# Kernel optimization log

Measured on AMD Instinct MI355X. Metric: run time of the kernel, lower is better.

Reference implementation:

```python
import jax, jax.numpy as jnp
import numpy as np

def setup_inputs() -> dict:
    key = jax.random.key(0)
    k1, k2, k3 = jax.random.split(key, 3)
    shape = (2, 2048, 8, 64)  # [n, l, h, d]
    return {
        "q": jax.random.normal(k1, shape, dtype=jnp.float32),
        "k": jax.random.normal(k2, shape, dtype=jnp.float32),
        "v": jax.random.normal(k3, shape, dtype=jnp.float32),
    }

def reference(q, k, v):
    # QK^T: [n, l, s, h]
    qk = jnp.einsum('nlhd,nshd->nlsh', q, k)
    softmax_temp = 1.0 / (q.shape[3] ** 0.5)
    attn = jax.nn.softmax(softmax_temp * qk, axis=2)
    # weighted values: [n, l, h, d]
    return jnp.einsum('nlsh,nshd->nlhd', attn, v)
```

## Files before the change

### kernel.cpp

```cpp
#include <hip/hip_runtime.h>
#include <hip/hip_bf16.h>
#include <math.h>

typedef float floatx16 __attribute__((ext_vector_type(16)));
typedef __bf16 bf16x8 __attribute__((ext_vector_type(8)));

#define SEQ 2048
#define NH 8
#define DH 64
#define NB 2
#define HEADS 16
#define HSTRIDE (SEQ * DH)
#define TILE_E (64 * 64)

__device__ __forceinline__ unsigned short f2bf(float x) {
  union { __bf16 b; unsigned short u; } c; c.b = (__bf16)x; return c.u;
}
__device__ __forceinline__ unsigned int pk2bf(float a, float b) {
  union { __hip_bfloat162 h2; unsigned int u; } c;
  c.h2 = __float22bfloat162_rn(make_float2(a, b));
  return c.u;
}

__device__ __forceinline__ void hswap_fwd(unsigned& a, unsigned& b) {
  asm volatile("v_permlane32_swap_b32 %0, %1" : "+v"(a), "+v"(b));
}
__device__ __forceinline__ void hswap_rev(unsigned& a, unsigned& b) {
  asm volatile("v_permlane32_swap_b32 %0, %1" : "+v"(b), "+v"(a));
}

__global__ __launch_bounds__(256)
void pack_kv(const float* __restrict__ k, const float* __restrict__ v,
             unsigned short* __restrict__ kb, unsigned short* __restrict__ vb) {
  __shared__ unsigned short Ts[64][68];
  const int tid  = threadIdx.x;
  const int bx   = blockIdx.x;
  const int head = bx & 15;
  const int kt   = bx >> 4;
  const int n = head >> 3, h = head & 7;

  #pragma unroll
  for (int j2 = 0; j2 < 2; ++j2) {
    int c = j2 * 256 + tid;
    int lane = c & 63;
    int kk = (c >> 6) & 3, ks2 = c >> 8;
    int row = kt * 64 + ks2 * 32 + (lane & 31);
    int d0  = kk * 16 + (lane >> 5) * 8;
    const float* src = k + ((size_t)(n * SEQ + row) * NH + h) * DH + d0;
    float4 a = *(const float4*)src;
    float4 b = *(const float4*)(src + 4);
    ushort4 lo, hi;
    lo.x = f2bf(a.x); lo.y = f2bf(a.y); lo.z = f2bf(a.z); lo.w = f2bf(a.w);
    hi.x = f2bf(b.x); hi.y = f2bf(b.y); hi.z = f2bf(b.z); hi.w = f2bf(b.w);
    unsigned short* dst = kb + (size_t)head * HSTRIDE + kt * TILE_E + c * 8;
    *(ushort4*)dst = lo;
    *(ushort4*)(dst + 4) = hi;
  }

  #pragma unroll
  for (int i = 0; i < 4; ++i) {
    int id = i * 256 + tid;
    int s  = id >> 4;
    int c4 = (id & 15) * 4;
    size_t g = ((size_t)((n * SEQ + kt * 64 + s) * NH + h)) * DH + c4;
    float4 x = *(const float4*)(v + g);
    ushort4 y;
    y.x = f2bf(x.x); y.y = f2bf(x.y); y.z = f2bf(x.z); y.w = f2bf(x.w);
    *(ushort4*)&Ts[s][c4] = y;
  }
  __syncthreads();
  #pragma unroll
  for (int j2 = 0; j2 < 2; ++j2) {
    int c = j2 * 256 + tid;
    int lane = c & 63;
    int dsub = (c >> 6) & 1, ss = c >> 7;
    int s0 = ss * 16 + (lane >> 5) * 8;
    int d  = dsub * 32 + (lane & 31);
    ushort4 lo, hi;
    lo.x = Ts[s0 + 0][d]; lo.y = Ts[s0 + 1][d]; lo.z = Ts[s0 + 2][d]; lo.w = Ts[s0 + 3][d];
    hi.x = Ts[s0 + 4][d]; hi.y = Ts[s0 + 5][d]; hi.z = Ts[s0 + 6][d]; hi.w = Ts[s0 + 7][d];
    unsigned short* dst = vb + (size_t)head * HSTRIDE + kt * TILE_E + c * 8;
    *(ushort4*)dst = lo;
    *(ushort4*)(dst + 4) = hi;
  }
}

#define SMEM_BYTES 37376

__global__ __launch_bounds__(512)
void attn(const float* __restrict__ q, const unsigned short* __restrict__ kb,
          const unsigned short* __restrict__ vt, float* __restrict__ out) {
  __shared__ __align__(16) char smem[SMEM_BYTES];
  float* oM = (float*)smem;
  float* lM = (float*)(smem + 8 * 16 * 72 * 4);

  const int tid  = threadIdx.x;
  const int wave = tid >> 6;
  const int lane = tid & 63;
  const int l32  = lane & 31;
  const int hl   = lane >> 5;
  const int wq   = wave >> 2;
  const int wk   = wave & 3;

  unsigned px = (unsigned)lane, py = (unsigned)lane + 100u;
  hswap_fwd(px, py);
  const bool mir = (__builtin_amdgcn_readfirstlane(px) != 0u);

  const int bx   = blockIdx.x;
  const int head = bx & 15;
  const int qh2  = bx >> 4;
  const int n = head >> 3, h = head & 7;

  const unsigned short* kf = kb + (size_t)head * HSTRIDE;
  const unsigned short* vf = vt + (size_t)head * HSTRIDE;

  bf16x8 qB[2][4];
  #pragma unroll
  for (int qs = 0; qs < 2; ++qs)
    #pragma unroll
    for (int kk = 0; kk < 4; ++kk) {
      const int row = qh2 * 128 + wq * 64 + qs * 32 + l32;
      const float* src = q + ((size_t)((n * SEQ + row) * NH + h)) * DH + kk * 16 + hl * 8;
      float4 x0 = *(const float4*)src;
      float4 x1 = *(const float4*)(src + 4);
      union { unsigned int u32[4]; bf16x8 v8; } u;
      u.u32[0] = pk2bf(x0.x, x0.y); u.u32[1] = pk2bf(x0.z, x0.w);
      u.u32[2] = pk2bf(x1.x, x1.y); u.u32[3] = pk2bf(x1.z, x1.w);
      qB[qs][kk] = u.v8;
    }

  floatx16 o[2][2];
  float lsum[2];
  #pragma unroll
  for (int qs = 0; qs < 2; ++qs) {
    lsum[qs] = 0.f;
    #pragma unroll
    for (int d = 0; d < 2; ++d)
      #pragma unroll
      for (int i = 0; i < 16; ++i) o[qs][d][i] = 0.f;
  }

  const float S = 0.125f * 1.4426950408889634f;
  const float C = 12.0f;

  for (int it = 0; it < 8; ++it) {
    const int kt = wk * 8 + it;
    const unsigned short* kt_base = kf + kt * TILE_E;
    const unsigned short* vt_base = vf + kt * TILE_E;

    bf16x8 kA[2][4];
    #pragma unroll
    for (int ks2 = 0; ks2 < 2; ++ks2)
      #pragma unroll
      for (int kk = 0; kk < 4; ++kk)
        kA[ks2][kk] = *(const bf16x8*)(kt_base + ((ks2 * 4 + kk) * 64 + lane) * 8);
    bf16x8 vB[4][2];
    #pragma unroll
    for (int ss = 0; ss < 4; ++ss)
      #pragma unroll
      for (int dsub = 0; dsub < 2; ++dsub)
        vB[ss][dsub] = *(const bf16x8*)(vt_base + ((ss * 2 + dsub) * 64 + lane) * 8);

    #pragma unroll
    for (int ks2 = 0; ks2 < 2; ++ks2) {
      floatx16 acc2[2];
      #pragma unroll
      for (int i = 0; i < 16; ++i) acc2[0][i] = 0.f;
      #pragma unroll
      for (int kk = 0; kk < 4; ++kk)
        acc2[0] = __builtin_amdgcn_mfma_f32_32x32x16_bf16(kA[ks2][kk], qB[0][kk], acc2[0], 0, 0, 0);

      #pragma unroll
      for (int m = 0; m < 2; ++m) {
        unsigned pk[8];
        #pragma unroll
        for (int g2 = 0; g2 < 4; ++g2) {
          float p0 = __builtin_amdgcn_exp2f(acc2[m][4 * g2 + 0] * S - C);
          float p1 = __builtin_amdgcn_exp2f(acc2[m][4 * g2 + 1] * S - C);
          float p2 = __builtin_amdgcn_exp2f(acc2[m][4 * g2 + 2] * S - C);
          float p3 = __builtin_amdgcn_exp2f(acc2[m][4 * g2 + 3] * S - C);
          lsum[m] += (p0 + p1) + (p2 + p3);
          pk[g2 * 2]     = pk2bf(p0, p1);
          pk[g2 * 2 + 1] = pk2bf(p2, p3);
        }

        if (m == 0) {
          #pragma unroll
          for (int i = 0; i < 16; ++i) acc2[1][i] = 0.f;
          #pragma unroll
          for (int kk = 0; kk < 4; ++kk)
            acc2[1] = __builtin_amdgcn_mfma_f32_32x32x16_bf16(kA[ks2][kk], qB[1][kk], acc2[1], 0, 0, 0);
        }

        union { unsigned u32[4]; bf16x8 v8; } A1, A2;
        A1.u32[0] = pk[0]; A1.u32[2] = pk[2];
        A1.u32[1] = pk[1]; A1.u32[3] = pk[3];
        A2.u32[0] = pk[4]; A2.u32[2] = pk[6];
        A2.u32[1] = pk[5]; A2.u32[3] = pk[7];
        if (!mir) {
          hswap_fwd(A1.u32[0], A1.u32[2]); hswap_fwd(A1.u32[1], A1.u32[3]);
          hswap_fwd(A2.u32[0], A2.u32[2]); hswap_fwd(A2.u32[1], A2.u32[3]);
        } else {
          hswap_rev(A1.u32[0], A1.u32[2]); hswap_rev(A1.u32[1], A1.u32[3]);
          hswap_rev(A2.u32[0], A2.u32[2]); hswap_rev(A2.u32[1], A2.u32[3]);
        }

        o[m][0] = __builtin_amdgcn_mfma_f32_32x32x16_bf16(A1.v8, vB[ks2 * 2][0],     o[m][0], 0, 0, 0);
        o[m][1] = __builtin_amdgcn_mfma_f32_32x32x16_bf16(A1.v8, vB[ks2 * 2][1],     o[m][1], 0, 0, 0);
        o[m][0] = __builtin_amdgcn_mfma_f32_32x32x16_bf16(A2.v8, vB[ks2 * 2 + 1][0], o[m][0], 0, 0, 0);
        o[m][1] = __builtin_amdgcn_mfma_f32_32x32x16_bf16(A2.v8, vB[ks2 * 2 + 1][1], o[m][1], 0, 0, 0);
      }
    }
  }

  #pragma unroll
  for (int qs = 0; qs < 2; ++qs)
    lsum[qs] += __shfl_xor(lsum[qs], 32, 64);

  const int r32  = tid >> 4;
  const int wqr  = r32 >> 4;
  const int prow = r32 & 15;
  const int col4 = tid & 15;
  #pragma unroll
  for (int p = 0; p < 4; ++p) {
    const int qsub = p >> 1, rh = p & 1;
    __syncthreads();
    #pragma unroll
    for (int r8 = 0; r8 < 8; ++r8) {
      const int r   = rh * 8 + r8;
      const int rip = (r8 & 3) + 4 * hl + 8 * (r8 >> 2);
      oM[(wave * 16 + rip) * 72 + l32]      = o[qsub][0][r];
      oM[(wave * 16 + rip) * 72 + 32 + l32] = o[qsub][1][r];
    }
    if (lane < 32 && ((lane >> 4) & 1) == rh) lM[wave * 16 + (lane & 15)] = lsum[qsub];
    __syncthreads();
    float4 s = make_float4(0.f, 0.f, 0.f, 0.f);
    float l = 0.f;
    #pragma unroll
    for (int j = 0; j < 4; ++j) {
      const int w = wqr * 4 + j;
      float4 t4 = *(const float4*)&oM[(w * 16 + prow) * 72 + col4 * 4];
      s.x += t4.x; s.y += t4.y; s.z += t4.z; s.w += t4.w;
      l += lM[w * 16 + prow];
    }
    float inv = 1.f / l;
    const int grow = qh2 * 128 + wqr * 64 + p * 16 + prow;
    float4 st; st.x = s.x * inv; st.y = s.y * inv; st.z = s.z * inv; st.w = s.w * inv;
    *(float4*)(out + ((size_t)((n * SEQ + grow) * NH + h)) * DH + col4 * 4) = st;
  }
}

extern "C" void kernel_launch(void* const* d_in, const int* in_sizes, int n_in,
                              void* d_out, int out_size, void* d_ws, size_t ws_size,
                              hipStream_t stream) {
  const float* q = (const float*)d_in[0];
  const float* k = (const float*)d_in[1];
  const float* v = (const float*)d_in[2];
  float* out = (float*)d_out;
  (void)in_sizes; (void)n_in; (void)out_size; (void)ws_size;

  unsigned short* kb = (unsigned short*)d_ws;
  unsigned short* vb = kb + (size_t)HEADS * HSTRIDE;

  pack_kv<<<HEADS * (SEQ / 64), 256, 0, stream>>>(k, v, kb, vb);
  attn<<<HEADS * (SEQ / 128), 512, 0, stream>>>(q, kb, vb, out);
}
```

Measured before the change: 100.1 us.

## Fuse K/V bf16 packing into attention kernel and drop pack pre-pass

Removes the separate pack_kv kernel and its workspace round trip. The attention kernel now reads fp32 K and V straight from the input layout and converts them to bf16 MFMA fragments in registers. V is gathered with eight strided scalar loads per fragment. This saves one launch and a full write and re-read of packed K/V. The cost is that every attention block re-reads and re-converts fp32 K/V for its head, which doubles load bytes per tile and adds conversion ALU work inside the main loop.

Result: slower. 116.5 us (+16.4%).

```diff
diff --git a/kernel.cpp b/kernel.cpp
--- a/kernel.cpp
+++ b/kernel.cpp
@@ -8,14 +8,9 @@
 #define SEQ 2048
 #define NH 8
 #define DH 64
-#define NB 2
 #define HEADS 16
-#define HSTRIDE (SEQ * DH)
-#define TILE_E (64 * 64)
-
-__device__ __forceinline__ unsigned short f2bf(float x) {
-  union { __bf16 b; unsigned short u; } c; c.b = (__bf16)x; return c.u;
-}
+#define RS (NH * DH)
+
 __device__ __forceinline__ unsigned int pk2bf(float a, float b) {
   union { __hip_bfloat162 h2; unsigned int u; } c;
   c.h2 = __float22bfloat162_rn(make_float2(a, b));
@@ -29,67 +24,11 @@
   asm volatile("v_permlane32_swap_b32 %0, %1" : "+v"(b), "+v"(a));
 }
 
-__global__ __launch_bounds__(256)
-void pack_kv(const float* __restrict__ k, const float* __restrict__ v,
-             unsigned short* __restrict__ kb, unsigned short* __restrict__ vb) {
-  __shared__ unsigned short Ts[64][68];
-  const int tid  = threadIdx.x;
-  const int bx   = blockIdx.x;
-  const int head = bx & 15;
-  const int kt   = bx >> 4;
-  const int n = head >> 3, h = head & 7;
-
-  #pragma unroll
-  for (int j2 = 0; j2 < 2; ++j2) {
-    int c = j2 * 256 + tid;
-    int lane = c & 63;
-    int kk = (c >> 6) & 3, ks2 = c >> 8;
-    int row = kt * 64 + ks2 * 32 + (lane & 31);
-    int d0  = kk * 16 + (lane >> 5) * 8;
-    const float* src = k + ((size_t)(n * SEQ + row) * NH + h) * DH + d0;
-    float4 a = *(const float4*)src;
-    float4 b = *(const float4*)(src + 4);
-    ushort4 lo, hi;
-    lo.x = f2bf(a.x); lo.y = f2bf(a.y); lo.z = f2bf(a.z); lo.w = f2bf(a.w);
-    hi.x = f2bf(b.x); hi.y = f2bf(b.y); hi.z = f2bf(b.z); hi.w = f2bf(b.w);
-    unsigned short* dst = kb + (size_t)head * HSTRIDE + kt * TILE_E + c * 8;
-    *(ushort4*)dst = lo;
-    *(ushort4*)(dst + 4) = hi;
-  }
-
-  #pragma unroll
-  for (int i = 0; i < 4; ++i) {
-    int id = i * 256 + tid;
-    int s  = id >> 4;
-    int c4 = (id & 15) * 4;
-    size_t g = ((size_t)((n * SEQ + kt * 64 + s) * NH + h)) * DH + c4;
-    float4 x = *(const float4*)(v + g);
-    ushort4 y;
-    y.x = f2bf(x.x); y.y = f2bf(x.y); y.z = f2bf(x.z); y.w = f2bf(x.w);
-    *(ushort4*)&Ts[s][c4] = y;
-  }
-  __syncthreads();
-  #pragma unroll
-  for (int j2 = 0; j2 < 2; ++j2) {
-    int c = j2 * 256 + tid;
-    int lane = c & 63;
-    int dsub = (c >> 6) & 1, ss = c >> 7;
-    int s0 = ss * 16 + (lane >> 5) * 8;
-    int d  = dsub * 32 + (lane & 31);
-    ushort4 lo, hi;
-    lo.x = Ts[s0 + 0][d]; lo.y = Ts[s0 + 1][d]; lo.z = Ts[s0 + 2][d]; lo.w = Ts[s0 + 3][d];
-    hi.x = Ts[s0 + 4][d]; hi.y = Ts[s0 + 5][d]; hi.z = Ts[s0 + 6][d]; hi.w = Ts[s0 + 7][d];
-    unsigned short* dst = vb + (size_t)head * HSTRIDE + kt * TILE_E + c * 8;
-    *(ushort4*)dst = lo;
-    *(ushort4*)(dst + 4) = hi;
-  }
-}
-
 #define SMEM_BYTES 37376
 
 __global__ __launch_bounds__(512)
-void attn(const float* __restrict__ q, const unsigned short* __restrict__ kb,
-          const unsigned short* __restrict__ vt, float* __restrict__ out) {
+void attn(const float* __restrict__ q, const float* __restrict__ k,
+          const float* __restrict__ v, float* __restrict__ out) {
   __shared__ __align__(16) char smem[SMEM_BYTES];
   float* oM = (float*)smem;
   float* lM = (float*)(smem + 8 * 16 * 72 * 4);
@@ -111,8 +50,8 @@
   const int qh2  = bx >> 4;
   const int n = head >> 3, h = head & 7;
 
-  const unsigned short* kf = kb + (size_t)head * HSTRIDE;
-  const unsigned short* vf = vt + (size_t)head * HSTRIDE;
+  const float* kf = k + ((size_t)n * SEQ * NH + h) * DH;
+  const float* vf = v + ((size_t)n * SEQ * NH + h) * DH;
 
   bf16x8 qB[2][4];
   #pragma unroll
@@ -145,21 +84,35 @@
 
   for (int it = 0; it < 8; ++it) {
     const int kt = wk * 8 + it;
-    const unsigned short* kt_base = kf + kt * TILE_E;
-    const unsigned short* vt_base = vf + kt * TILE_E;
+    const float* kt_base = kf + (size_t)kt * 64 * RS;
+    const float* vt_base = vf + (size_t)kt * 64 * RS;
 
     bf16x8 kA[2][4];
     #pragma unroll
     for (int ks2 = 0; ks2 < 2; ++ks2)
       #pragma unroll
-      for (int kk = 0; kk < 4; ++kk)
-        kA[ks2][kk] = *(const bf16x8*)(kt_base + ((ks2 * 4 + kk) * 64 + lane) * 8);
+      for (int kk = 0; kk < 4; ++kk) {
+        const float* src = kt_base + (size_t)(ks2 * 32 + l32) * RS + kk * 16 + hl * 8;
+        float4 x0 = *(const float4*)src;
+        float4 x1 = *(const float4*)(src + 4);
+        union { unsigned int u32[4]; bf16x8 v8; } u;
+        u.u32[0] = pk2bf(x0.x, x0.y); u.u32[1] = pk2bf(x0.z, x0.w);
+        u.u32[2] = pk2bf(x1.x, x1.y); u.u32[3] = pk2bf(x1.z, x1.w);
+        kA[ks2][kk] = u.v8;
+      }
     bf16x8 vB[4][2];
     #pragma unroll
     for (int ss = 0; ss < 4; ++ss)
       #pragma unroll
-      for (int dsub = 0; dsub < 2; ++dsub)
-        vB[ss][dsub] = *(const bf16x8*)(vt_base + ((ss * 2 + dsub) * 64 + lane) * 8);
+      for (int dsub = 0; dsub < 2; ++dsub) {
+        const float* src = vt_base + (size_t)(ss * 16 + hl * 8) * RS + dsub * 32 + l32;
+        float w0 = src[0 * RS], w1 = src[1 * RS], w2 = src[2 * RS], w3 = src[3 * RS];
+        float w4 = src[4 * RS], w5 = src[5 * RS], w6 = src[6 * RS], w7 = src[7 * RS];
+        union { unsigned int u32[4]; bf16x8 v8; } u;
+        u.u32[0] = pk2bf(w0, w1); u.u32[1] = pk2bf(w2, w3);
+        u.u32[2] = pk2bf(w4, w5); u.u32[3] = pk2bf(w6, w7);
+        vB[ss][dsub] = u.v8;
+      }
 
     #pragma unroll
     for (int ks2 = 0; ks2 < 2; ++ks2) {
@@ -257,11 +210,7 @@
   const float* k = (const float*)d_in[1];
   const float* v = (const float*)d_in[2];
   float* out = (float*)d_out;
-  (void)in_sizes; (void)n_in; (void)out_size; (void)ws_size;
-
-  unsigned short* kb = (unsigned short*)d_ws;
-  unsigned short* vb = kb + (size_t)HEADS * HSTRIDE;
-
-  pack_kv<<<HEADS * (SEQ / 64), 256, 0, stream>>>(k, v, kb, vb);
-  attn<<<HEADS * (SEQ / 128), 512, 0, stream>>>(q, kb, vb, out);
-}
+  (void)in_sizes; (void)n_in; (void)out_size; (void)d_ws; (void)ws_size;
+
+  attn<<<HEADS * (SEQ / 128), 512, 0, stream>>>(q, k, v, out);
+}
```

## Split attention into smaller 32-query blocks with four waves for more occupancy

Applied to the files above, without the earlier changes.

Each block now handles 32 query rows using four waves that split the key sequence, instead of 128 rows across eight waves. This quadruples the grid and lowers per-wave register use to raise occupancy and latency hiding across CUs. K/V tile loads are also staggered within each iteration to overlap with MFMA work. In exchange, each K/V tile fetched is reused for fewer queries, increasing L2/global traffic.

New measurement: 111.7 us. 1.12x slower.

```diff
diff --git a/kernel.cpp b/kernel.cpp
--- a/kernel.cpp
+++ b/kernel.cpp
@@ -85,22 +85,20 @@
   }
 }
 
-#define SMEM_BYTES 37376
-
-__global__ __launch_bounds__(512)
+#define SMEM_BYTES (4 * 16 * 72 * 4 + 4 * 16 * 4)
+
+__global__ __launch_bounds__(256, 4)
 void attn(const float* __restrict__ q, const unsigned short* __restrict__ kb,
           const unsigned short* __restrict__ vt, float* __restrict__ out) {
   __shared__ __align__(16) char smem[SMEM_BYTES];
   float* oM = (float*)smem;
-  float* lM = (float*)(smem + 8 * 16 * 72 * 4);
+  float* lM = (float*)(smem + 4 * 16 * 72 * 4);
 
   const int tid  = threadIdx.x;
   const int wave = tid >> 6;
   const int lane = tid & 63;
   const int l32  = lane & 31;
   const int hl   = lane >> 5;
-  const int wq   = wave >> 2;
-  const int wk   = wave & 3;
 
   unsigned px = (unsigned)lane, py = (unsigned)lane + 100u;
   hswap_fwd(px, py);
@@ -108,143 +106,161 @@
 
   const int bx   = blockIdx.x;
   const int head = bx & 15;
-  const int qh2  = bx >> 4;
+  const int qc   = bx >> 4;
   const int n = head >> 3, h = head & 7;
 
-  const unsigned short* kf = kb + (size_t)head * HSTRIDE;
-  const unsigned short* vf = vt + (size_t)head * HSTRIDE;
-
-  bf16x8 qB[2][4];
-  #pragma unroll
-  for (int qs = 0; qs < 2; ++qs)
-    #pragma unroll
-    for (int kk = 0; kk < 4; ++kk) {
-      const int row = qh2 * 128 + wq * 64 + qs * 32 + l32;
-      const float* src = q + ((size_t)((n * SEQ + row) * NH + h)) * DH + kk * 16 + hl * 8;
-      float4 x0 = *(const float4*)src;
-      float4 x1 = *(const float4*)(src + 4);
-      union { unsigned int u32[4]; bf16x8 v8; } u;
-      u.u32[0] = pk2bf(x0.x, x0.y); u.u32[1] = pk2bf(x0.z, x0.w);
-      u.u32[2] = pk2bf(x1.x, x1.y); u.u32[3] = pk2bf(x1.z, x1.w);
-      qB[qs][kk] = u.v8;
-    }
-
-  floatx16 o[2][2];
-  float lsum[2];
-  #pragma unroll
-  for (int qs = 0; qs < 2; ++qs) {
-    lsum[qs] = 0.f;
-    #pragma unroll
-    for (int d = 0; d < 2; ++d)
-      #pragma unroll
-      for (int i = 0; i < 16; ++i) o[qs][d][i] = 0.f;
-  }
+  const int swk = __builtin_amdgcn_readfirstlane(wave);
+  const unsigned short* kq = kb + (size_t)head * HSTRIDE + (size_t)swk * 8 * TILE_E;
+  const unsigned short* vq = vt + (size_t)head * HSTRIDE + (size_t)swk * 8 * TILE_E;
+
+  bf16x8 qB[4];
+  #pragma unroll
+  for (int kk = 0; kk < 4; ++kk) {
+    const int row = qc * 32 + l32;
+    const float* src = q + ((size_t)((n * SEQ + row) * NH + h)) * DH + kk * 16 + hl * 8;
+    float4 x0 = *(const float4*)src;
+    float4 x1 = *(const float4*)(src + 4);
+    union { unsigned int u32[4]; bf16x8 v8; } u;
+    u.u32[0] = pk2bf(x0.x, x0.y); u.u32[1] = pk2bf(x0.z, x0.w);
+    u.u32[2] = pk2bf(x1.x, x1.y); u.u32[3] = pk2bf(x1.z, x1.w);
+    qB[kk] = u.v8;
+  }
+
+  floatx16 o[2];
+  float lsum = 0.f;
+  #pragma unroll
+  for (int d = 0; d < 2; ++d)
+    #pragma unroll
+    for (int i = 0; i < 16; ++i) o[d][i] = 0.f;
 
   const float S = 0.125f * 1.4426950408889634f;
   const float C = 12.0f;
 
   for (int it = 0; it < 8; ++it) {
-    const int kt = wk * 8 + it;
-    const unsigned short* kt_base = kf + kt * TILE_E;
-    const unsigned short* vt_base = vf + kt * TILE_E;
-
-    bf16x8 kA[2][4];
-    #pragma unroll
-    for (int ks2 = 0; ks2 < 2; ++ks2)
-      #pragma unroll
-      for (int kk = 0; kk < 4; ++kk)
-        kA[ks2][kk] = *(const bf16x8*)(kt_base + ((ks2 * 4 + kk) * 64 + lane) * 8);
-    bf16x8 vB[4][2];
-    #pragma unroll
-    for (int ss = 0; ss < 4; ++ss)
-      #pragma unroll
-      for (int dsub = 0; dsub < 2; ++dsub)
-        vB[ss][dsub] = *(const bf16x8*)(vt_base + ((ss * 2 + dsub) * 64 + lane) * 8);
-
-    #pragma unroll
-    for (int ks2 = 0; ks2 < 2; ++ks2) {
-      floatx16 acc2[2];
-      #pragma unroll
-      for (int i = 0; i < 16; ++i) acc2[0][i] = 0.f;
-      #pragma unroll
-      for (int kk = 0; kk < 4; ++kk)
-        acc2[0] = __builtin_amdgcn_mfma_f32_32x32x16_bf16(kA[ks2][kk], qB[0][kk], acc2[0], 0, 0, 0);
-
-      #pragma unroll
-      for (int m = 0; m < 2; ++m) {
-        unsigned pk[8];
+    const unsigned short* tb_k = kq + it * TILE_E;
+    const unsigned short* tb_v = vq + it * TILE_E;
+
+    bf16x8 kA0[4], kA1[4];
+    bf16x8 vb0[2][2], vb1[2][2];
+    #pragma unroll
+    for (int kk = 0; kk < 4; ++kk)
+      kA0[kk] = *(const bf16x8*)(tb_k + (kk * 64 + lane) * 8);
+    #pragma unroll
+    for (int j = 0; j < 2; ++j)
+      #pragma unroll
+      for (int d = 0; d < 2; ++d)
+        vb0[j][d] = *(const bf16x8*)(tb_v + ((j * 2 + d) * 64 + lane) * 8);
+    #pragma unroll
+    for (int kk = 0; kk < 4; ++kk)
+      kA1[kk] = *(const bf16x8*)(tb_k + ((4 + kk) * 64 + lane) * 8);
+
+    floatx16 acc;
+    #pragma unroll
+    for (int i = 0; i < 16; ++i) acc[i] = 0.f;
+    #pragma unroll
+    for (int kk = 0; kk < 4; ++kk)
+      acc = __builtin_amdgcn_mfma_f32_32x32x16_bf16(kA0[kk], qB[kk], acc, 0, 0, 0);
+
+    {
+      unsigned pkv[8];
+      #pragma unroll
+      for (int g2 = 0; g2 < 4; ++g2) {
+        float p0 = __builtin_amdgcn_exp2f(acc[4 * g2 + 0] * S - C);
+        float p1 = __builtin_amdgcn_exp2f(acc[4 * g2 + 1] * S - C);
+        float p2 = __builtin_amdgcn_exp2f(acc[4 * g2 + 2] * S - C);
+        float p3 = __builtin_amdgcn_exp2f(acc[4 * g2 + 3] * S - C);
+        lsum += (p0 + p1) + (p2 + p3);
+        pkv[g2 * 2]     = pk2bf(p0, p1);
+        pkv[g2 * 2 + 1] = pk2bf(p2, p3);
+      }
+      #pragma unroll
+      for (int j = 0; j < 2; ++j)
         #pragma unroll
-        for (int g2 = 0; g2 < 4; ++g2) {
-          float p0 = __builtin_amdgcn_exp2f(acc2[m][4 * g2 + 0] * S - C);
-          float p1 = __builtin_amdgcn_exp2f(acc2[m][4 * g2 + 1] * S - C);
-          float p2 = __builtin_amdgcn_exp2f(acc2[m][4 * g2 + 2] * S - C);
-          float p3 = __builtin_amdgcn_exp2f(acc2[m][4 * g2 + 3] * S - C);
-          lsum[m] += (p0 + p1) + (p2 + p3);
-          pk[g2 * 2]     = pk2bf(p0, p1);
-          pk[g2 * 2 + 1] = pk2bf(p2, p3);
-        }
-
-        if (m == 0) {
-          #pragma unroll
-          for (int i = 0; i < 16; ++i) acc2[1][i] = 0.f;
-          #pragma unroll
-          for (int kk = 0; kk < 4; ++kk)
-            acc2[1] = __builtin_amdgcn_mfma_f32_32x32x16_bf16(kA[ks2][kk], qB[1][kk], acc2[1], 0, 0, 0);
-        }
-
-        union { unsigned u32[4]; bf16x8 v8; } A1, A2;
-        A1.u32[0] = pk[0]; A1.u32[2] = pk[2];
-        A1.u32[1] = pk[1]; A1.u32[3] = pk[3];
-        A2.u32[0] = pk[4]; A2.u32[2] = pk[6];
-        A2.u32[1] = pk[5]; A2.u32[3] = pk[7];
-        if (!mir) {
-          hswap_fwd(A1.u32[0], A1.u32[2]); hswap_fwd(A1.u32[1], A1.u32[3]);
-          hswap_fwd(A2.u32[0], A2.u32[2]); hswap_fwd(A2.u32[1], A2.u32[3]);
-        } else {
-          hswap_rev(A1.u32[0], A1.u32[2]); hswap_rev(A1.u32[1], A1.u32[3]);
-          hswap_rev(A2.u32[0], A2.u32[2]); hswap_rev(A2.u32[1], A2.u32[3]);
-        }
-
-        o[m][0] = __builtin_amdgcn_mfma_f32_32x32x16_bf16(A1.v8, vB[ks2 * 2][0],     o[m][0], 0, 0, 0);
-        o[m][1] = __builtin_amdgcn_mfma_f32_32x32x16_bf16(A1.v8, vB[ks2 * 2][1],     o[m][1], 0, 0, 0);
-        o[m][0] = __builtin_amdgcn_mfma_f32_32x32x16_bf16(A2.v8, vB[ks2 * 2 + 1][0], o[m][0], 0, 0, 0);
-        o[m][1] = __builtin_amdgcn_mfma_f32_32x32x16_bf16(A2.v8, vB[ks2 * 2 + 1][1], o[m][1], 0, 0, 0);
-      }
-    }
-  }
-
-  #pragma unroll
-  for (int qs = 0; qs < 2; ++qs)
-    lsum[qs] += __shfl_xor(lsum[qs], 32, 64);
-
-  const int r32  = tid >> 4;
-  const int wqr  = r32 >> 4;
-  const int prow = r32 & 15;
+        for (int d = 0; d < 2; ++d)
+          vb1[j][d] = *(const bf16x8*)(tb_v + (((2 + j) * 2 + d) * 64 + lane) * 8);
+
+      union { unsigned u32[4]; bf16x8 v8; } A1, A2;
+      A1.u32[0] = pkv[0]; A1.u32[2] = pkv[2];
+      A1.u32[1] = pkv[1]; A1.u32[3] = pkv[3];
+      A2.u32[0] = pkv[4]; A2.u32[2] = pkv[6];
+      A2.u32[1] = pkv[5]; A2.u32[3] = pkv[7];
+      if (!mir) {
+        hswap_fwd(A1.u32[0], A1.u32[2]); hswap_fwd(A1.u32[1], A1.u32[3]);
+        hswap_fwd(A2.u32[0], A2.u32[2]); hswap_fwd(A2.u32[1], A2.u32[3]);
+      } else {
+        hswap_rev(A1.u32[0], A1.u32[2]); hswap_rev(A1.u32[1], A1.u32[3]);
+        hswap_rev(A2.u32[0], A2.u32[2]); hswap_rev(A2.u32[1], A2.u32[3]);
+      }
+      o[0] = __builtin_amdgcn_mfma_f32_32x32x16_bf16(A1.v8, vb0[0][0], o[0], 0, 0, 0);
+      o[1] = __builtin_amdgcn_mfma_f32_32x32x16_bf16(A1.v8, vb0[0][1], o[1], 0, 0, 0);
+      o[0] = __builtin_amdgcn_mfma_f32_32x32x16_bf16(A2.v8, vb0[1][0], o[0], 0, 0, 0);
+      o[1] = __builtin_amdgcn_mfma_f32_32x32x16_bf16(A2.v8, vb0[1][1], o[1], 0, 0, 0);
+    }
+
+    #pragma unroll
+    for (int i = 0; i < 16; ++i) acc[i] = 0.f;
+    #pragma unroll
+    for (int kk = 0; kk < 4; ++kk)
+      acc = __builtin_amdgcn_mfma_f32_32x32x16_bf16(kA1[kk], qB[kk], acc, 0, 0, 0);
+
+    {
+      unsigned pkv[8];
+      #pragma unroll
+      for (int g2 = 0; g2 < 4; ++g2) {
+        float p0 = __builtin_amdgcn_exp2f(acc[4 * g2 + 0] * S - C);
+        float p1 = __builtin_amdgcn_exp2f(acc[4 * g2 + 1] * S - C);
+        float p2 = __builtin_amdgcn_exp2f(acc[4 * g2 + 2] * S - C);
+        float p3 = __builtin_amdgcn_exp2f(acc[4 * g2 + 3] * S - C);
+        lsum += (p0 + p1) + (p2 + p3);
+        pkv[g2 * 2]     = pk2bf(p0, p1);
+        pkv[g2 * 2 + 1] = pk2bf(p2, p3);
+      }
+      union { unsigned u32[4]; bf16x8 v8; } A1, A2;
+      A1.u32[0] = pkv[0]; A1.u32[2] = pkv[2];
+      A1.u32[1] = pkv[1]; A1.u32[3] = pkv[3];
+      A2.u32[0] = pkv[4]; A2.u32[2] = pkv[6];
+      A2.u32[1] = pkv[5]; A2.u32[3] = pkv[7];
+      if (!mir) {
+        hswap_fwd(A1.u32[0], A1.u32[2]); hswap_fwd(A1.u32[1], A1.u32[3]);
+        hswap_fwd(A2.u32[0], A2.u32[2]); hswap_fwd(A2.u32[1], A2.u32[3]);
+      } else {
+        hswap_rev(A1.u32[0], A1.u32[2]); hswap_rev(A1.u32[1], A1.u32[3]);
+        hswap_rev(A2.u32[0], A2.u32[2]); hswap_rev(A2.u32[1], A2.u32[3]);
+      }
+      o[0] = __builtin_amdgcn_mfma_f32_32x32x16_bf16(A1.v8, vb1[0][0], o[0], 0, 0, 0);
+      o[1] = __builtin_amdgcn_mfma_f32_32x32x16_bf16(A1.v8, vb1[0][1], o[1], 0, 0, 0);
+      o[0] = __builtin_amdgcn_mfma_f32_32x32x16_bf16(A2.v8, vb1[1][0], o[0], 0, 0, 0);
+      o[1] = __builtin_amdgcn_mfma_f32_32x32x16_bf16(A2.v8, vb1[1][1], o[1], 0, 0, 0);
+    }
+  }
+
+  lsum += __shfl_xor(lsum, 32, 64);
+
+  const int prow = tid >> 4;
   const int col4 = tid & 15;
   #pragma unroll
-  for (int p = 0; p < 4; ++p) {
-    const int qsub = p >> 1, rh = p & 1;
+  for (int p = 0; p < 2; ++p) {
+    const int rh = p;
     __syncthreads();
     #pragma unroll
     for (int r8 = 0; r8 < 8; ++r8) {
       const int r   = rh * 8 + r8;
       const int rip = (r8 & 3) + 4 * hl + 8 * (r8 >> 2);
-      oM[(wave * 16 + rip) * 72 + l32]      = o[qsub][0][r];
-      oM[(wave * 16 + rip) * 72 + 32 + l32] = o[qsub][1][r];
-    }
-    if (lane < 32 && ((lane >> 4) & 1) == rh) lM[wave * 16 + (lane & 15)] = lsum[qsub];
+      oM[(wave * 16 + rip) * 72 + l32]      = o[0][r];
+      oM[(wave * 16 + rip) * 72 + 32 + l32] = o[1][r];
+    }
+    if (lane < 32 && ((lane >> 4) & 1) == rh) lM[wave * 16 + (lane & 15)] = lsum;
     __syncthreads();
     float4 s = make_float4(0.f, 0.f, 0.f, 0.f);
     float l = 0.f;
     #pragma unroll
-    for (int j = 0; j < 4; ++j) {
-      const int w = wqr * 4 + j;
+    for (int w = 0; w < 4; ++w) {
       float4 t4 = *(const float4*)&oM[(w * 16 + prow) * 72 + col4 * 4];
       s.x += t4.x; s.y += t4.y; s.z += t4.z; s.w += t4.w;
       l += lM[w * 16 + prow];
     }
     float inv = 1.f / l;
-    const int grow = qh2 * 128 + wqr * 64 + p * 16 + prow;
+    const int grow = qc * 32 + p * 16 + prow;
     float4 st; st.x = s.x * inv; st.y = s.y * inv; st.z = s.z * inv; st.w = s.w * inv;
     *(float4*)(out + ((size_t)((n * SEQ + grow) * NH + h)) * DH + col4 * 4) = st;
   }
@@ -263,5 +279,5 @@
   unsigned short* vb = kb + (size_t)HEADS * HSTRIDE;
 
   pack_kv<<<HEADS * (SEQ / 64), 256, 0, stream>>>(k, v, kb, vb);
-  attn<<<HEADS * (SEQ / 128), 512, 0, stream>>>(q, kb, vb, out);
-}
+  attn<<<HEADS * (SEQ / 32), 256, 0, stream>>>(q, kb, vb, out);
+}
```
